# Kernel optimization log

Hardware: AMD Instinct MI355X
Metric: run time of the kernel (lower is better)

## Reference

```python
import jax, jax.numpy as jnp
import numpy as np

IMSIZE = 2048
LINEWIDTH = 7  # odd, >1


def gen_kernel(linewidth=LINEWIDTH):
    # Pyramid-shaped smoothing kernel, same as RenderNet.gen_kernel
    center = linewidth // 2
    k = np.zeros((3, 3, linewidth, linewidth), dtype=np.float32)
    for i in range(center + 1):
        width = linewidth - 2 * i
        value = (i + 1) / float(center + 1)
        off = (linewidth - width) // 2
        k[:, :, off:linewidth - off, off:linewidth - off] = value
    return jnp.asarray(k)


def setup_inputs() -> dict:
    return {
        "x0": jnp.array([100.0], jnp.float32),
        "y0": jnp.array([200.0], jnp.float32),
        "x1": jnp.array([1800.0], jnp.float32),
        "y1": jnp.array([1500.0], jnp.float32),
        "kernel": gen_kernel(),
    }


def reference(x0, y0, x1, y1, kernel):
    n = IMSIZE
    x0s, y0s, x1s, y1s = x0[0], y0[0], x1[0], y1[0]
    dx = jnp.abs(x1s - x0s)
    dy = jnp.abs(y1s - y0s)
    sx = jnp.where(x1s > x0s, 1.0, -1.0)
    sy = jnp.where(y1s > y0s, 1.0, -1.0)
    steep = dy > dx
    # swap axes if steep (x0<->y0, dx<->dy, sx<->sy), matching the torch code
    X = jnp.where(steep, y0s, x0s)
    Y = jnp.where(steep, x0s, y0s)
    DX = jnp.where(steep, dy, dx)
    DY = jnp.where(steep, dx, dy)
    SX = jnp.where(steep, sy, sx)
    SY = jnp.where(steep, sx, sy)
    n_iter = jnp.floor(DX).astype(jnp.int32)  # range(0, int(dx)), dx >= 0

    def step(carry, i):
        x, y, d = carry
        active = (i < n_iter).astype(jnp.float32)
        # mat2vecidx(a, b) = n*b + a; steep uses (y0, x0), else (x0, y0)
        idx = jnp.where(steep, n * x + y, n * y + x).astype(jnp.int32)
        # the torch `while d >= 0` body executes at most once per iteration
        move = (d >= 0).astype(x.dtype)
        y = y + SY * move
        d = d - 2.0 * DX * move
        x = x + SX
        d = d + 2.0 * DY
        return (x, y, d), (idx, active)

    d0 = 2.0 * DY - DX
    _, (idxs, actives) = jax.lax.scan(step, (X, Y, d0), jnp.arange(n, dtype=jnp.int32))
    idxs = jnp.clip(idxs, 0, n * n - 1)
    template = jnp.zeros((n * n,), jnp.float32).at[idxs].max(actives)
    end_idx = jnp.clip((n * y1s + x1s).astype(jnp.int32), 0, n * n - 1)
    template = template.at[end_idx].set(1.0)

    img = jnp.broadcast_to(template.reshape(n, n)[None, None], (1, 3, n, n))
    pad = LINEWIDTH // 2
    out = jax.lax.conv_general_dilated(
        img, kernel, window_strides=(1, 1), padding=[(pad, pad), (pad, pad)],
        dimension_numbers=("NCHW", "OIHW", "NCHW"))
    tmin = out.min()
    tmax = out.max()
    return (out - tmin) / (tmax - tmin)
```

## Files before the change

### kernel.cpp

```cpp
#include <hip/hip_runtime.h>
#include <math.h>

#define N 2048
#define NN (N * N)
#define TAPS 49
#define ORANGE 17
#define MAXCAND ((N + 7) * ORANGE)
#define CAND_BLOCKS ((MAXCAND + 255) / 256)

typedef float f4 __attribute__((ext_vector_type(4)));


struct LineP {
    int steep, X0, Y0, SX, SY, DX, DY, cnt, ex, ey;
};

__device__ inline LineP load_params(const float* x0p, const float* y0p,
                                    const float* x1p, const float* y1p) {
    float x0s = x0p[0], y0s = y0p[0], x1s = x1p[0], y1s = y1p[0];
    float dxf = fabsf(x1s - x0s), dyf = fabsf(y1s - y0s);
    bool steep = dyf > dxf;
    float sx = (x1s > x0s) ? 1.f : -1.f;
    float sy = (y1s > y0s) ? 1.f : -1.f;
    LineP p;
    p.steep = steep;
    p.X0 = (int)(steep ? y0s : x0s);
    p.Y0 = (int)(steep ? x0s : y0s);
    p.DX = (int)(steep ? dyf : dxf);
    p.DY = (int)(steep ? dxf : dyf);
    p.SX = (int)(steep ? sy : sx);
    p.SY = (int)(steep ? sx : sy);
    p.cnt = p.DX < N ? p.DX : N;
    int e = (int)((float)N * y1s + x1s);
    e = e < 0 ? 0 : (e > NN - 1 ? NN - 1 : e);
    p.ey = e >> 11;
    p.ex = e & (N - 1);
    return p;
}

__device__ inline int line_m(const LineP& p, int i) {
    return (int)((unsigned)(2 * p.DY * i + p.DX) / (unsigned)(2 * p.DX));
}

__device__ inline void cand_pixel(const LineP& p, int e, int& r, int& c) {
    int ii = e / ORANGE - 3;
    int o = e - (ii + 3) * ORANGE - 8;
    int d = p.X0 + ii * p.SX;
    int icl = ii < 0 ? 0 : (ii > p.cnt - 1 ? p.cnt - 1 : ii);
    int m = p.cnt > 0 ? line_m(p, icl) : 0;
    int u = p.Y0 + m * p.SY + o;
    r = p.steep ? d : u;
    c = p.steep ? u : d;
}

__device__ inline float conv_at(const LineP& p, int r, int c, const float* keff) {
    int t = p.steep ? r : c;
    int u = p.steep ? c : r;
    float w = 0.f;
    if (p.cnt > 0) {
        int icen = (t - p.X0) * p.SX;
        if (icen >= -3 && icen <= p.cnt + 2) {
            int ilo = icen - 3 < 0 ? 0 : icen - 3;
            int ihi = icen + 3 > p.cnt - 1 ? p.cnt - 1 : icen + 3;
            for (int i = ilo; i <= ihi; ++i) {
                int m = line_m(p, i);
                int other = p.Y0 + m * p.SY;
                int d_other = u - other;
                if (d_other >= -3 && d_other <= 3) {
                    int d_drive = (icen - i) * p.SX;
                    int d_row = p.steep ? d_drive : d_other;
                    int d_col = p.steep ? d_other : d_drive;
                    w += keff[(3 - d_row) * 7 + (3 - d_col)];
                }
            }
        }
    }
    int dr = r - p.ey, dc = c - p.ex;
    if (dr >= -3 && dr <= 3 && dc >= -3 && dc <= 3)
        w += keff[(3 - dr) * 7 + (3 - dc)];
    return w;
}

__global__ void __launch_bounds__(256)
k_fill_tmax(const float* x0p, const float* y0p, const float* x1p, const float* y1p,
            const float* __restrict__ kern, int* __restrict__ tmax_bits,
            float* __restrict__ out) {
    int gid = blockIdx.x * blockDim.x + threadIdx.x;
    f4 z = {0.f, 0.f, 0.f, 0.f};
    f4* o4 = (f4*)out;
    const int Q = NN / 4;
    __builtin_nontemporal_store(z, &o4[gid]);
    __builtin_nontemporal_store(z, &o4[gid + Q]);
    __builtin_nontemporal_store(z, &o4[gid + 2 * Q]);

    if (blockIdx.x < CAND_BLOCKS) {
        __shared__ float keff[TAPS];
        __shared__ float smax[4];
        if (threadIdx.x < TAPS)
            keff[threadIdx.x] = kern[threadIdx.x] + kern[TAPS + threadIdx.x]
                              + kern[2 * TAPS + threadIdx.x];
        __syncthreads();
        LineP p = load_params(x0p, y0p, x1p, y1p);
        int total = (p.cnt + 7) * ORANGE;
        float v = 0.f;
        if (gid < total) {
            int r, c;
            cand_pixel(p, gid, r, c);
            if ((unsigned)r < (unsigned)N && (unsigned)c < (unsigned)N)
                v = conv_at(p, r, c, keff);
        }
        for (int off = 32; off; off >>= 1)
            v = fmaxf(v, __shfl_down(v, off));
        int wave = threadIdx.x >> 6, lane = threadIdx.x & 63;
        if (lane == 0) smax[wave] = v;
        __syncthreads();
        if (threadIdx.x == 0) {
            v = fmaxf(fmaxf(smax[0], smax[1]), fmaxf(smax[2], smax[3]));
            atomicMax(tmax_bits, __float_as_int(v));
        }
    }
}

__global__ void __launch_bounds__(256)
k_band(const float* x0p, const float* y0p, const float* x1p, const float* y1p,
       const float* __restrict__ kern, const int* __restrict__ tmax_bits,
       float* __restrict__ out) {
    __shared__ float keff[TAPS];
    if (threadIdx.x < TAPS)
        keff[threadIdx.x] = kern[threadIdx.x] + kern[TAPS + threadIdx.x]
                          + kern[2 * TAPS + threadIdx.x];
    __syncthreads();
    LineP p = load_params(x0p, y0p, x1p, y1p);
    float scale = 1.f / __int_as_float(*tmax_bits);
    int e = blockIdx.x * blockDim.x + threadIdx.x;
    int total = (p.cnt + 7) * ORANGE;
    if (e >= total) return;
    int r, c;
    cand_pixel(p, e, r, c);
    if ((unsigned)r < (unsigned)N && (unsigned)c < (unsigned)N) {
        float w = conv_at(p, r, c, keff) * scale;
        int idx = r * N + c;
        out[idx] = w;
        out[idx + NN] = w;
        out[idx + 2 * NN] = w;
    }
}

extern "C" void kernel_launch(void* const* d_in, const int* in_sizes, int n_in,
                              void* d_out, int out_size, void* d_ws, size_t ws_size,
                              hipStream_t stream) {
    const float* x0 = (const float*)d_in[0];
    const float* y0 = (const float*)d_in[1];
    const float* x1 = (const float*)d_in[2];
    const float* y1 = (const float*)d_in[3];
    const float* kern = (const float*)d_in[4];
    float* out = (float*)d_out;
    int* tmax_bits = (int*)d_ws;

    k_fill_tmax<<<NN / 4 / 256, 256, 0, stream>>>(x0, y0, x1, y1, kern, tmax_bits, out);
    k_band<<<CAND_BLOCKS, 256, 0, stream>>>(x0, y0, x1, y1, kern, tmax_bits, out);
}
```

Before: 17.19 us.

## Fuse zero-fill, max reduction and band write into one kernel with grid sync

Merges the fill/max kernel and the band kernel into a single launch. Band-covering quads are excluded from the zero-fill by a predicate and written exactly once with vectorised f4 stores. The first CB blocks publish per-block maxima with magic-flag handshakes and spin-wait on each other, replacing the second launch with an in-kernel barrier. This removes a kernel launch and the double writes, but it relies on all CB blocks being co-resident and on a MAGIC flag in workspace that is never cleared between calls, so a stale flag could let a block read an old maximum.

```diff
diff --git a/kernel.cpp b/kernel.cpp
--- a/kernel.cpp
+++ b/kernel.cpp
@@ -5,14 +5,16 @@
 #define NN (N * N)
 #define TAPS 49
 #define ORANGE 17
-#define MAXCAND ((N + 7) * ORANGE)
-#define CAND_BLOCKS ((MAXCAND + 255) / 256)
+#define CB 137
+#define MAGIC 0x5AFE600D
+#define GRID (NN / 4 / 256)
 
 typedef float f4 __attribute__((ext_vector_type(4)));
 
 
 struct LineP {
     int steep, X0, Y0, SX, SY, DX, DY, cnt, ex, ey;
+    float X0f, Y0f, SYf, SXf, slope;
 };
 
 __device__ inline LineP load_params(const float* x0p, const float* y0p,
@@ -35,6 +37,11 @@
     e = e < 0 ? 0 : (e > NN - 1 ? NN - 1 : e);
     p.ey = e >> 11;
     p.ex = e & (N - 1);
+    p.X0f = (float)p.X0;
+    p.Y0f = (float)p.Y0;
+    p.SXf = (float)p.SX;
+    p.SYf = (float)p.SY;
+    p.slope = p.DX > 0 ? (float)p.DY / (float)p.DX : 0.f;
     return p;
 }
 
@@ -81,68 +88,125 @@
     return w;
 }
 
+__device__ __attribute__((noinline)) bool quadP(const LineP& p, int r, int c0) {
+    if (r >= p.ey - 3 && r <= p.ey + 3 && c0 <= p.ex + 3 && c0 + 3 >= p.ex - 3)
+        return true;
+    if (p.cnt <= 0) return false;
+    if (!p.steep) {
+        float ic = ((float)c0 + 1.5f - p.X0f) * p.SXf;
+        if (ic < -5.0f || ic > (float)p.cnt + 4.0f) return false;
+        float est = p.Y0f + p.SYf * p.slope * ic;
+        return fabsf((float)r - est) <= 8.5f;
+    } else {
+        float ic = ((float)r - p.X0f) * p.SXf;
+        if (ic < -3.5f || ic > (float)p.cnt + 2.5f) return false;
+        float est = p.Y0f + p.SYf * p.slope * ic;
+        return ((float)c0 <= est + 7.0f) && ((float)(c0 + 3) >= est - 7.0f);
+    }
+}
+
 __global__ void __launch_bounds__(256)
-k_fill_tmax(const float* x0p, const float* y0p, const float* x1p, const float* y1p,
-            const float* __restrict__ kern, int* __restrict__ tmax_bits,
-            float* __restrict__ out) {
-    int gid = blockIdx.x * blockDim.x + threadIdx.x;
-    f4 z = {0.f, 0.f, 0.f, 0.f};
+k_fused(const float* x0p, const float* y0p, const float* x1p, const float* y1p,
+        const float* __restrict__ kern, int* __restrict__ ws,
+        float* __restrict__ out) {
+    const int tid = threadIdx.x, bid = blockIdx.x;
+    const int gid = bid * 256 + tid;
+    const int Q = NN / 4;
+    LineP p = load_params(x0p, y0p, x1p, y1p);
     f4* o4 = (f4*)out;
-    const int Q = NN / 4;
-    __builtin_nontemporal_store(z, &o4[gid]);
-    __builtin_nontemporal_store(z, &o4[gid + Q]);
-    __builtin_nontemporal_store(z, &o4[gid + 2 * Q]);
-
-    if (blockIdx.x < CAND_BLOCKS) {
-        __shared__ float keff[TAPS];
-        __shared__ float smax[4];
-        if (threadIdx.x < TAPS)
-            keff[threadIdx.x] = kern[threadIdx.x] + kern[TAPS + threadIdx.x]
-                              + kern[2 * TAPS + threadIdx.x];
-        __syncthreads();
-        LineP p = load_params(x0p, y0p, x1p, y1p);
-        int total = (p.cnt + 7) * ORANGE;
-        float v = 0.f;
-        if (gid < total) {
-            int r, c;
-            cand_pixel(p, gid, r, c);
-            if ((unsigned)r < (unsigned)N && (unsigned)c < (unsigned)N)
-                v = conv_at(p, r, c, keff);
+
+    {
+        int pix = gid << 2;
+        int r = pix >> 11, c0 = pix & (N - 1);
+        if (!quadP(p, r, c0)) {
+            f4 z = {0.f, 0.f, 0.f, 0.f};
+            __builtin_nontemporal_store(z, &o4[gid]);
+            __builtin_nontemporal_store(z, &o4[gid + Q]);
+            __builtin_nontemporal_store(z, &o4[gid + 2 * Q]);
         }
-        for (int off = 32; off; off >>= 1)
-            v = fmaxf(v, __shfl_down(v, off));
-        int wave = threadIdx.x >> 6, lane = threadIdx.x & 63;
-        if (lane == 0) smax[wave] = v;
-        __syncthreads();
-        if (threadIdx.x == 0) {
-            v = fmaxf(fmaxf(smax[0], smax[1]), fmaxf(smax[2], smax[3]));
-            atomicMax(tmax_bits, __float_as_int(v));
+    }
+    if (bid >= CB) return;
+
+    __shared__ float keff[TAPS];
+    __shared__ float sred[4];
+    __shared__ float stmax;
+    if (tid < TAPS)
+        keff[tid] = kern[tid] + kern[TAPS + tid] + kern[2 * TAPS + tid];
+    __syncthreads();
+
+    float v = 0.f;
+    int totalc = (p.cnt + 7) * ORANGE;
+    if (gid < totalc) {
+        int r, c;
+        cand_pixel(p, gid, r, c);
+        if ((unsigned)r < (unsigned)N && (unsigned)c < (unsigned)N)
+            v = conv_at(p, r, c, keff);
+    }
+    for (int off = 32; off; off >>= 1) v = fmaxf(v, __shfl_down(v, off));
+    if ((tid & 63) == 0) sred[tid >> 6] = v;
+    __syncthreads();
+    if (tid == 0) {
+        v = fmaxf(fmaxf(sred[0], sred[1]), fmaxf(sred[2], sred[3]));
+        atomicExch(&ws[bid], __float_as_int(v));
+        __threadfence();
+        atomicExch(&ws[256 + bid], MAGIC);
+    }
+
+    float pv = 0.f;
+    if (tid < CB) {
+        while (atomicAdd(&ws[256 + tid], 0) != MAGIC)
+            __builtin_amdgcn_s_sleep(2);
+        __threadfence();
+        pv = __int_as_float(atomicAdd(&ws[tid], 0));
+    }
+    for (int off = 32; off; off >>= 1) pv = fmaxf(pv, __shfl_down(pv, off));
+    __syncthreads();
+    if ((tid & 63) == 0) sred[tid >> 6] = pv;
+    __syncthreads();
+    if (tid == 0)
+        stmax = fmaxf(fmaxf(sred[0], sred[1]), fmaxf(sred[2], sred[3]));
+    __syncthreads();
+    float scale = 1.f / stmax;
+
+    int r2 = -1, c02 = -1;
+    if (gid < 21) {
+        r2 = p.ey - 3 + gid / 3;
+        c02 = ((p.ex - 3) & ~3) + 4 * (gid % 3);
+    } else if (p.cnt > 0) {
+        int li = gid - 21;
+        if (!p.steep) {
+            int tend = p.X0 + p.cnt * p.SX;
+            int cmin = (p.X0 < tend ? p.X0 : tend) - 7;
+            int cmax = (p.X0 > tend ? p.X0 : tend) + 4;
+            int cbase = cmin & ~3;
+            int nq = ((cmax - cbase) >> 2) + 1;
+            int k = li / 19, dr = li - k * 19;
+            if (k < nq) {
+                c02 = cbase + 4 * k;
+                float ic = ((float)c02 + 1.5f - p.X0f) * p.SXf;
+                float est = p.Y0f + p.SYf * p.slope * ic;
+                r2 = (int)floorf(est) - 9 + dr;
+            }
+        } else {
+            int k = li / 5, j = li - k * 5;
+            if (k <= p.cnt + 6) {
+                r2 = p.X0 + (k - 3) * p.SX;
+                float ic = (float)((r2 - p.X0) * p.SX);
+                float est = p.Y0f + p.SYf * p.slope * ic;
+                c02 = ((((int)floorf(est) - 10) & ~3)) + 4 * j;
+            }
         }
     }
-}
-
-__global__ void __launch_bounds__(256)
-k_band(const float* x0p, const float* y0p, const float* x1p, const float* y1p,
-       const float* __restrict__ kern, const int* __restrict__ tmax_bits,
-       float* __restrict__ out) {
-    __shared__ float keff[TAPS];
-    if (threadIdx.x < TAPS)
-        keff[threadIdx.x] = kern[threadIdx.x] + kern[TAPS + threadIdx.x]
-                          + kern[2 * TAPS + threadIdx.x];
-    __syncthreads();
-    LineP p = load_params(x0p, y0p, x1p, y1p);
-    float scale = 1.f / __int_as_float(*tmax_bits);
-    int e = blockIdx.x * blockDim.x + threadIdx.x;
-    int total = (p.cnt + 7) * ORANGE;
-    if (e >= total) return;
-    int r, c;
-    cand_pixel(p, e, r, c);
-    if ((unsigned)r < (unsigned)N && (unsigned)c < (unsigned)N) {
-        float w = conv_at(p, r, c, keff) * scale;
-        int idx = r * N + c;
-        out[idx] = w;
-        out[idx + NN] = w;
-        out[idx + 2 * NN] = w;
+    if (r2 >= 0 && r2 < N && c02 >= 0 && c02 <= N - 4 && quadP(p, r2, c02)) {
+        f4 w;
+        w.x = conv_at(p, r2, c02,     keff) * scale;
+        w.y = conv_at(p, r2, c02 + 1, keff) * scale;
+        w.z = conv_at(p, r2, c02 + 2, keff) * scale;
+        w.w = conv_at(p, r2, c02 + 3, keff) * scale;
+        int qid = (r2 << 9) + (c02 >> 2);
+        __builtin_nontemporal_store(w, &o4[qid]);
+        __builtin_nontemporal_store(w, &o4[qid + Q]);
+        __builtin_nontemporal_store(w, &o4[qid + 2 * Q]);
     }
 }
 
@@ -154,9 +218,6 @@
     const float* x1 = (const float*)d_in[2];
     const float* y1 = (const float*)d_in[3];
     const float* kern = (const float*)d_in[4];
-    float* out = (float*)d_out;
-    int* tmax_bits = (int*)d_ws;
-
-    k_fill_tmax<<<NN / 4 / 256, 256, 0, stream>>>(x0, y0, x1, y1, kern, tmax_bits, out);
-    k_band<<<CAND_BLOCKS, 256, 0, stream>>>(x0, y0, x1, y1, kern, tmax_bits, out);
-}
+    k_fused<<<GRID, 256, 0, stream>>>(x0, y0, x1, y1, kern, (int*)d_ws,
+                                      (float*)d_out);
+}
```

New measurement: 49.55 us. 2.88x slower.
